# Kernel tuning notes

Measured on AMD Instinct MI355X. Metric: run time of the kernel, lower is better.

Reference implementation:

```python
import jax, jax.numpy as jnp
import numpy as np


def setup_inputs() -> dict:
    key = jax.random.key(0)
    kq, kk, kv = jax.random.split(key, 3)
    B, H, S, D = 4, 16, 2048, 64
    q = jax.random.normal(kq, (B, H, S, D), dtype=jnp.float32)
    k = jax.random.normal(kk, (B, H, S, D), dtype=jnp.float32)
    v = jax.random.normal(kv, (B, H, S, D), dtype=jnp.float32)
    return {"q": q, "k": k, "v": v}


def reference(q, k, v):
    # Flash-attention math (causal=True, softmax_scale = 1/sqrt(head_dim)).
    D = q.shape[-1]
    scale = 1.0 / np.sqrt(D).astype(np.float32)
    # scores: [B, H, Sq, Sk]
    scores = jnp.einsum('bhqd,bhkd->bhqk', q, k) * scale
    Sq, Sk = scores.shape[-2], scores.shape[-1]
    causal_mask = jnp.tril(jnp.ones((Sq, Sk), dtype=bool))  # [Sq, Sk]
    neg_inf = jnp.asarray(jnp.finfo(scores.dtype).min, scores.dtype)
    scores = jnp.where(causal_mask, scores, neg_inf)
    probs = jax.nn.softmax(scores, axis=-1)
    out = jnp.einsum('bhqk,bhkd->bhqd', probs, v)
    return out
```

## Files before the change

### kernel.cpp

```cpp
#include <hip/hip_runtime.h>
#include <hip/hip_bf16.h>

#define S_LEN 2048
#define DH 64
#define QBLK 128
#define KVBLK 64
#define LDPK 72
#define LDPV 68

typedef __attribute__((ext_vector_type(4)))  float f32x4;
typedef __attribute__((ext_vector_type(16))) float f32x16;
typedef __attribute__((ext_vector_type(8)))  short short8v;
typedef __attribute__((ext_vector_type(4)))  unsigned uint4v;
typedef __attribute__((ext_vector_type(2)))  unsigned uint2v;

__device__ __forceinline__ unsigned cvt_pk(float a, float b) {
    unsigned r;
    asm("v_cvt_pk_bf16_f32 %0, %1, %2" : "=v"(r) : "v"(a), "v"(b));
    return r;
}

__global__ __launch_bounds__(512) void fa_fwd_kernel(
    const float* __restrict__ Q, const float* __restrict__ K,
    const float* __restrict__ V, float* __restrict__ O)
{
    const int tid  = threadIdx.x;
    const int lane = tid & 63;
    const int w    = tid >> 6;
    const int bh   = blockIdx.x & 63;
    const int p    = blockIdx.x >> 6;

    const int qb = (w < 4) ? (15 - p) : p;
    const int q0 = qb * QBLK + (w & 3) * 32;
    const int kv_end = (16 - p) * QBLK;

    const size_t base = (size_t)bh * S_LEN * DH;
    const float* Qg = Q + base;
    const float* Kg = K + base;
    const float* Vg = V + base;
    float*       Og = O + base;

    __shared__ __align__(16) short K_lds[2][KVBLK][LDPK];
    __shared__ __align__(16) short V_lds[2][DH][LDPV];

    const int q  = lane & 31;
    const int hi = lane >> 5;
    const int kr = tid >> 3;
    const int dc = (tid & 7) * 8;
    const int vd = tid & 63;
    const int vg = tid >> 6;

    unsigned kpfu[4], vpf[4];

    auto prefetch = [&](int kvb) {
        const float* kp = Kg + (size_t)(kvb + kr) * DH + dc;
        f32x4 a = *(const f32x4*)kp;
        f32x4 b = *(const f32x4*)(kp + 4);
        kpfu[0] = cvt_pk(a[0], a[1]); kpfu[1] = cvt_pk(a[2], a[3]);
        kpfu[2] = cvt_pk(b[0], b[1]); kpfu[3] = cvt_pk(b[2], b[3]);
        #pragma unroll
        for (int i = 0; i < 4; ++i) {
            int kv = vg * 8 + i * 2;
            float x = Vg[(size_t)(kvb + kv) * DH + vd];
            float y = Vg[(size_t)(kvb + kv + 1) * DH + vd];
            vpf[i] = cvt_pk(x, y);
        }
    };

    auto stage = [&](int b) {
        uint4v u = {kpfu[0], kpfu[1], kpfu[2], kpfu[3]};
        *(uint4v*)&K_lds[b][kr][dc] = u;
        #pragma unroll
        for (int i = 0; i < 4; ++i) {
            int kv = vg * 8 + i * 2;
            *(unsigned*)((char*)&V_lds[b][0][0] + vd * (LDPV * 2) + kv * 2) = vpf[i];
        }
    };

    const float qscale = 0.125f * 1.44269504088896340736f;

    short8v qfrag[4];
    #pragma unroll
    for (int ds = 0; ds < 4; ++ds) {
        const float* qp = Qg + (size_t)(q0 + q) * DH + ds * 16 + hi * 8;
        f32x4 a = *(const f32x4*)qp;
        f32x4 b = *(const f32x4*)(qp + 4);
        uint4v u;
        u[0] = cvt_pk(a[0] * qscale, a[1] * qscale);
        u[1] = cvt_pk(a[2] * qscale, a[3] * qscale);
        u[2] = cvt_pk(b[0] * qscale, b[1] * qscale);
        u[3] = cvt_pk(b[2] * qscale, b[3] * qscale);
        qfrag[ds] = __builtin_bit_cast(short8v, u);
    }

    f32x16 o_acc[2];
    o_acc[0] = (f32x16)(0.f);
    o_acc[1] = (f32x16)(0.f);
    float m_run = -1e30f, l_run = 0.f;

    prefetch(0);
    stage(0);
    int cur = 0;
    __syncthreads();

    #pragma unroll 1
    for (int kvb = 0; kvb < kv_end; kvb += KVBLK) {
        int nkv = kvb + KVBLK;
        const bool have = nkv < kv_end;
        if (have) prefetch(nkv);

        if (kvb <= q0) {
            const short (*Kc)[LDPK] = K_lds[cur];
            const char* Vc = (const char*)&V_lds[cur][0][0];

            f32x16 s_acc[2];
            s_acc[0] = (f32x16)(0.f);
            s_acc[1] = (f32x16)(0.f);

            __builtin_amdgcn_s_setprio(1);
            #pragma unroll
            for (int ds = 0; ds < 4; ++ds) {
                #pragma unroll
                for (int kt = 0; kt < 2; ++kt) {
                    short8v kf = *(const short8v*)&Kc[kt * 32 + q][ds * 16 + hi * 8];
                    s_acc[kt] = __builtin_amdgcn_mfma_f32_32x32x16_bf16(
                        kf, qfrag[ds], s_acc[kt], 0, 0, 0);
                }
            }
            __builtin_amdgcn_s_setprio(0);

            const int qrow = q0 + q;
            if (kvb + KVBLK - 1 > q0) {
                #pragma unroll
                for (int kt = 0; kt < 2; ++kt)
                    #pragma unroll
                    for (int r = 0; r < 16; ++r) {
                        int kv = kvb + kt * 32 + (r & 3) + 8 * (r >> 2) + 4 * hi;
                        if (kv > qrow) s_acc[kt][r] = -1e30f;
                    }
            }

            float tl = -1e30f;
            #pragma unroll
            for (int kt = 0; kt < 2; ++kt)
                #pragma unroll
                for (int r = 0; r < 16; ++r)
                    tl = fmaxf(tl, s_acc[kt][r]);
            float tmax = fmaxf(tl, __shfl_xor(tl, 32));

            if (!__all(tmax <= m_run + 8.0f)) {
                float mnew = fmaxf(m_run, tmax);
                float corr = __builtin_amdgcn_exp2f(m_run - mnew);
                m_run = mnew;
                l_run *= corr;
                #pragma unroll
                for (int dt = 0; dt < 2; ++dt)
                    #pragma unroll
                    for (int r = 0; r < 16; ++r)
                        o_acc[dt][r] *= corr;
            }

            float rsum = 0.f;
            #pragma unroll
            for (int kt = 0; kt < 2; ++kt)
                #pragma unroll
                for (int r = 0; r < 16; ++r) {
                    float pe = __builtin_amdgcn_exp2f(s_acc[kt][r] - m_run);
                    s_acc[kt][r] = pe;
                    rsum += pe;
                }
            rsum += __shfl_xor(rsum, 32);
            l_run += rsum;

            unsigned pk_[2][8];
            #pragma unroll
            for (int kt = 0; kt < 2; ++kt)
                #pragma unroll
                for (int m = 0; m < 8; ++m)
                    pk_[kt][m] = cvt_pk(s_acc[kt][2 * m], s_acc[kt][2 * m + 1]);

            __builtin_amdgcn_s_setprio(1);
            #pragma unroll
            for (int s = 0; s < 4; ++s) {
                const int kt = s >> 1, bofs = 4 * (s & 1);
                uint4v bu = {pk_[kt][bofs], pk_[kt][bofs + 1],
                             pk_[kt][bofs + 2], pk_[kt][bofs + 3]};
                short8v pb = __builtin_bit_cast(short8v, bu);
                #pragma unroll
                for (int dt = 0; dt < 2; ++dt) {
                    const char* vrow = Vc + (size_t)(dt * 32 + q) * (LDPV * 2);
                    uint2v lo = *(const uint2v*)(vrow + (16 * s + 4 * hi) * 2);
                    uint2v h2 = *(const uint2v*)(vrow + (16 * s + 8 + 4 * hi) * 2);
                    uint4v au = {lo[0], lo[1], h2[0], h2[1]};
                    short8v va = __builtin_bit_cast(short8v, au);
                    o_acc[dt] = __builtin_amdgcn_mfma_f32_32x32x16_bf16(
                        va, pb, o_acc[dt], 0, 0, 0);
                }
            }
            __builtin_amdgcn_s_setprio(0);
        }

        if (have) {
            stage(cur ^ 1);
            __syncthreads();
        }
        cur ^= 1;
    }

    float inv = 1.0f / l_run;
    float* orow = Og + (size_t)(q0 + q) * DH;
    #pragma unroll
    for (int dt = 0; dt < 2; ++dt) {
        #pragma unroll
        for (int g = 0; g < 4; ++g) {
            f32x4 ov = {o_acc[dt][4 * g] * inv,     o_acc[dt][4 * g + 1] * inv,
                        o_acc[dt][4 * g + 2] * inv, o_acc[dt][4 * g + 3] * inv};
            *(f32x4*)(orow + dt * 32 + 8 * g + 4 * hi) = ov;
        }
    }
}

extern "C" void kernel_launch(void* const* d_in, const int* in_sizes, int n_in,
                              void* d_out, int out_size, void* d_ws, size_t ws_size,
                              hipStream_t stream) {
    const float* q = (const float*)d_in[0];
    const float* k = (const float*)d_in[1];
    const float* v = (const float*)d_in[2];
    float* out = (float*)d_out;
    fa_fwd_kernel<<<dim3(512), dim3(512), 0, stream>>>(q, k, v, out);
}
```

Before: 65.68 us.

## Permute V LDS layout for 128-bit reads, remap blocks, tree-reduce softmax

Widens the V LDS row pitch and stores V columns in a permuted order. Each MFMA A-fragment can then be fetched with a single 128-bit LDS read instead of two 64-bit reads, and staging uses two 64-bit writes instead of four 32-bit writes. The block-to-(bh, p) mapping is reordered so concurrently scheduled blocks pair light and heavy causal work differently and may share heads for cache locality. The softmax max and sum reductions become tree reductions to shorten dependency chains, at the cost of slightly more registers and a possible change in LDS bank conflicts.

```diff
diff --git a/kernel.cpp b/kernel.cpp
--- a/kernel.cpp
+++ b/kernel.cpp
@@ -6,7 +6,7 @@
 #define QBLK 128
 #define KVBLK 64
 #define LDPK 72
-#define LDPV 68
+#define LDPV 72
 
 typedef __attribute__((ext_vector_type(4)))  float f32x4;
 typedef __attribute__((ext_vector_type(16))) float f32x16;
@@ -18,6 +18,14 @@
     unsigned r;
     asm("v_cvt_pk_bf16_f32 %0, %1, %2" : "=v"(r) : "v"(a), "v"(b));
     return r;
+}
+
+__device__ __forceinline__ int vcol(int kv) {
+    int ss = kv >> 4, w16 = kv & 15;
+    int hi = (w16 >> 2) & 1;
+    int m  = w16 - 4 * hi;
+    int j  = (m & 3) + 4 * (m >> 3);
+    return ss * 16 + hi * 8 + j;
 }
 
 __global__ __launch_bounds__(512) void fa_fwd_kernel(
@@ -27,8 +35,10 @@
     const int tid  = threadIdx.x;
     const int lane = tid & 63;
     const int w    = tid >> 6;
-    const int bh   = blockIdx.x & 63;
-    const int p    = blockIdx.x >> 6;
+    const int bid  = blockIdx.x;
+    const int lo8  = (bid >> 5) & 7;
+    const int p    = (bid < 256) ? lo8 : 7 - lo8;
+    const int bh   = (bid & 31) | ((bid >> 8) << 5);
 
     const int qb = (w < 4) ? (15 - p) : p;
     const int q0 = qb * QBLK + (w & 3) * 32;
@@ -49,6 +59,8 @@
     const int dc = (tid & 7) * 8;
     const int vd = tid & 63;
     const int vg = tid >> 6;
+    const int c0 = vcol(vg * 8);
+    const int c1 = vcol(vg * 8 + 4);
 
     unsigned kpfu[4], vpf[4];
 
@@ -70,11 +82,10 @@
     auto stage = [&](int b) {
         uint4v u = {kpfu[0], kpfu[1], kpfu[2], kpfu[3]};
         *(uint4v*)&K_lds[b][kr][dc] = u;
-        #pragma unroll
-        for (int i = 0; i < 4; ++i) {
-            int kv = vg * 8 + i * 2;
-            *(unsigned*)((char*)&V_lds[b][0][0] + vd * (LDPV * 2) + kv * 2) = vpf[i];
-        }
+        uint2v v0 = {vpf[0], vpf[1]};
+        uint2v v1 = {vpf[2], vpf[3]};
+        *(uint2v*)&V_lds[b][vd][c0] = v0;
+        *(uint2v*)&V_lds[b][vd][c1] = v1;
     };
 
     const float qscale = 0.125f * 1.44269504088896340736f;
@@ -140,13 +151,16 @@
                     }
             }
 
-            float tl = -1e30f;
-            #pragma unroll
-            for (int kt = 0; kt < 2; ++kt)
-                #pragma unroll
-                for (int r = 0; r < 16; ++r)
-                    tl = fmaxf(tl, s_acc[kt][r]);
-            float tmax = fmaxf(tl, __shfl_xor(tl, 32));
+            float pm[16];
+            #pragma unroll
+            for (int r = 0; r < 16; ++r)
+                pm[r] = fmaxf(s_acc[0][r], s_acc[1][r]);
+            #pragma unroll
+            for (int st = 8; st >= 1; st >>= 1)
+                #pragma unroll
+                for (int r = 0; r < st; ++r)
+                    pm[r] = fmaxf(pm[r], pm[r + st]);
+            float tmax = fmaxf(pm[0], __shfl_xor(pm[0], 32));
 
             if (!__all(tmax <= m_run + 8.0f)) {
                 float mnew = fmaxf(m_run, tmax);
@@ -160,17 +174,21 @@
                         o_acc[dt][r] *= corr;
             }
 
-            float rsum = 0.f;
-            #pragma unroll
-            for (int kt = 0; kt < 2; ++kt)
-                #pragma unroll
-                for (int r = 0; r < 16; ++r) {
-                    float pe = __builtin_amdgcn_exp2f(s_acc[kt][r] - m_run);
-                    s_acc[kt][r] = pe;
-                    rsum += pe;
-                }
-            rsum += __shfl_xor(rsum, 32);
-            l_run += rsum;
+            float ps[16];
+            #pragma unroll
+            for (int r = 0; r < 16; ++r) {
+                float a = __builtin_amdgcn_exp2f(s_acc[0][r] - m_run);
+                float b = __builtin_amdgcn_exp2f(s_acc[1][r] - m_run);
+                s_acc[0][r] = a;
+                s_acc[1][r] = b;
+                ps[r] = a + b;
+            }
+            #pragma unroll
+            for (int st = 8; st >= 1; st >>= 1)
+                #pragma unroll
+                for (int r = 0; r < st; ++r)
+                    ps[r] += ps[r + st];
+            l_run += ps[0] + __shfl_xor(ps[0], 32);
 
             unsigned pk_[2][8];
             #pragma unroll
@@ -188,11 +206,8 @@
                 short8v pb = __builtin_bit_cast(short8v, bu);
                 #pragma unroll
                 for (int dt = 0; dt < 2; ++dt) {
-                    const char* vrow = Vc + (size_t)(dt * 32 + q) * (LDPV * 2);
-                    uint2v lo = *(const uint2v*)(vrow + (16 * s + 4 * hi) * 2);
-                    uint2v h2 = *(const uint2v*)(vrow + (16 * s + 8 + 4 * hi) * 2);
-                    uint4v au = {lo[0], lo[1], h2[0], h2[1]};
-                    short8v va = __builtin_bit_cast(short8v, au);
+                    short8v va = *(const short8v*)(Vc +
+                        (size_t)(dt * 32 + q) * (LDPV * 2) + (16 * s + 8 * hi) * 2);
                     o_acc[dt] = __builtin_amdgcn_mfma_f32_32x32x16_bf16(
                         va, pb, o_acc[dt], 0, 0, 0);
                 }
```

Measured after the change: 75.96 us. 1.16x slower.

## Split KV tiles across wave pairs and merge partial softmax states in LDS

Applied to the files above, without the earlier changes.

Doubles the grid so each block handles half of each paired Q tile. Waves are split by parity so that each wave pair processes alternating KV tiles for the same 32 query rows. The two partial (m, l, O) states are then merged through shared memory reused as a merge buffer. The aim is more parallelism and shorter per-wave serial KV loops. The cost is that every block now streams the full KV range for only half the queries, which doubles K/V global loads and LDS staging, plus an extra merge step.

```diff
diff --git a/kernel.cpp b/kernel.cpp
--- a/kernel.cpp
+++ b/kernel.cpp
@@ -28,11 +28,16 @@
     const int lane = tid & 63;
     const int w    = tid >> 6;
     const int bh   = blockIdx.x & 63;
-    const int p    = blockIdx.x >> 6;
-
-    const int qb = (w < 4) ? (15 - p) : p;
-    const int q0 = qb * QBLK + (w & 3) * 32;
+    const int pp   = blockIdx.x >> 6;
+    const int p    = pp & 7;
+    const int half = pp >> 3;
+
+    const int u    = w & 3;
+    const int par  = w >> 2;
+    const int qb   = (u < 2) ? (15 - p) : p;
+    const int q0   = qb * QBLK + half * 64 + (u & 1) * 32;
     const int kv_end = (16 - p) * QBLK;
+    const int T    = kv_end >> 6;
 
     const size_t base = (size_t)bh * S_LEN * DH;
     const float* Qg = Q + base;
@@ -40,8 +45,10 @@
     const float* Vg = V + base;
     float*       Og = O + base;
 
-    __shared__ __align__(16) short K_lds[2][KVBLK][LDPK];
-    __shared__ __align__(16) short V_lds[2][DH][LDPV];
+    __shared__ __align__(16) char smem[35840];
+    short (*K_lds)[KVBLK][LDPK] = (short(*)[KVBLK][LDPK])smem;
+    short (*V_lds)[DH][LDPV]    = (short(*)[DH][LDPV])(smem + 18432);
+    float (*Mbuf)[64][34]       = (float(*)[64][34])smem;
 
     const int q  = lane & 31;
     const int hi = lane >> 5;
@@ -68,8 +75,8 @@
     };
 
     auto stage = [&](int b) {
-        uint4v u = {kpfu[0], kpfu[1], kpfu[2], kpfu[3]};
-        *(uint4v*)&K_lds[b][kr][dc] = u;
+        uint4v uu = {kpfu[0], kpfu[1], kpfu[2], kpfu[3]};
+        *(uint4v*)&K_lds[b][kr][dc] = uu;
         #pragma unroll
         for (int i = 0; i < 4; ++i) {
             int kv = vg * 8 + i * 2;
@@ -85,12 +92,12 @@
         const float* qp = Qg + (size_t)(q0 + q) * DH + ds * 16 + hi * 8;
         f32x4 a = *(const f32x4*)qp;
         f32x4 b = *(const f32x4*)(qp + 4);
-        uint4v u;
-        u[0] = cvt_pk(a[0] * qscale, a[1] * qscale);
-        u[1] = cvt_pk(a[2] * qscale, a[3] * qscale);
-        u[2] = cvt_pk(b[0] * qscale, b[1] * qscale);
-        u[3] = cvt_pk(b[2] * qscale, b[3] * qscale);
-        qfrag[ds] = __builtin_bit_cast(short8v, u);
+        uint4v uu;
+        uu[0] = cvt_pk(a[0] * qscale, a[1] * qscale);
+        uu[1] = cvt_pk(a[2] * qscale, a[3] * qscale);
+        uu[2] = cvt_pk(b[0] * qscale, b[1] * qscale);
+        uu[3] = cvt_pk(b[2] * qscale, b[3] * qscale);
+        qfrag[ds] = __builtin_bit_cast(short8v, uu);
     }
 
     f32x16 o_acc[2];
@@ -98,107 +105,109 @@
     o_acc[1] = (f32x16)(0.f);
     float m_run = -1e30f, l_run = 0.f;
 
+    auto computeTile = [&](int cur, int kvb) {
+        const short (*Kc)[LDPK] = K_lds[cur];
+        const char* Vc = (const char*)&V_lds[cur][0][0];
+
+        f32x16 s_acc[2];
+        s_acc[0] = (f32x16)(0.f);
+        s_acc[1] = (f32x16)(0.f);
+
+        __builtin_amdgcn_s_setprio(1);
+        #pragma unroll
+        for (int ds = 0; ds < 4; ++ds) {
+            #pragma unroll
+            for (int kt = 0; kt < 2; ++kt) {
+                short8v kf = *(const short8v*)&Kc[kt * 32 + q][ds * 16 + hi * 8];
+                s_acc[kt] = __builtin_amdgcn_mfma_f32_32x32x16_bf16(
+                    kf, qfrag[ds], s_acc[kt], 0, 0, 0);
+            }
+        }
+        __builtin_amdgcn_s_setprio(0);
+
+        const int qrow = q0 + q;
+        if (kvb + KVBLK - 1 > q0) {
+            #pragma unroll
+            for (int kt = 0; kt < 2; ++kt)
+                #pragma unroll
+                for (int r = 0; r < 16; ++r) {
+                    int kv = kvb + kt * 32 + (r & 3) + 8 * (r >> 2) + 4 * hi;
+                    if (kv > qrow) s_acc[kt][r] = -1e30f;
+                }
+        }
+
+        float tl = -1e30f;
+        #pragma unroll
+        for (int kt = 0; kt < 2; ++kt)
+            #pragma unroll
+            for (int r = 0; r < 16; ++r)
+                tl = fmaxf(tl, s_acc[kt][r]);
+        float tmax = fmaxf(tl, __shfl_xor(tl, 32));
+
+        if (!__all(tmax <= m_run + 8.0f)) {
+            float mnew = fmaxf(m_run, tmax);
+            float corr = __builtin_amdgcn_exp2f(m_run - mnew);
+            m_run = mnew;
+            l_run *= corr;
+            #pragma unroll
+            for (int dt = 0; dt < 2; ++dt)
+                #pragma unroll
+                for (int r = 0; r < 16; ++r)
+                    o_acc[dt][r] *= corr;
+        }
+
+        float rsum = 0.f;
+        #pragma unroll
+        for (int kt = 0; kt < 2; ++kt)
+            #pragma unroll
+            for (int r = 0; r < 16; ++r) {
+                float pe = __builtin_amdgcn_exp2f(s_acc[kt][r] - m_run);
+                s_acc[kt][r] = pe;
+                rsum += pe;
+            }
+        rsum += __shfl_xor(rsum, 32);
+        l_run += rsum;
+
+        unsigned pk_[2][8];
+        #pragma unroll
+        for (int kt = 0; kt < 2; ++kt)
+            #pragma unroll
+            for (int m = 0; m < 8; ++m)
+                pk_[kt][m] = cvt_pk(s_acc[kt][2 * m], s_acc[kt][2 * m + 1]);
+
+        __builtin_amdgcn_s_setprio(1);
+        #pragma unroll
+        for (int ss = 0; ss < 4; ++ss) {
+            const int kt = ss >> 1, bofs = 4 * (ss & 1);
+            uint4v bu = {pk_[kt][bofs], pk_[kt][bofs + 1],
+                         pk_[kt][bofs + 2], pk_[kt][bofs + 3]};
+            short8v pb = __builtin_bit_cast(short8v, bu);
+            #pragma unroll
+            for (int dt = 0; dt < 2; ++dt) {
+                const char* vrow = Vc + (size_t)(dt * 32 + q) * (LDPV * 2);
+                uint2v lo = *(const uint2v*)(vrow + (16 * ss + 4 * hi) * 2);
+                uint2v h2 = *(const uint2v*)(vrow + (16 * ss + 8 + 4 * hi) * 2);
+                uint4v au = {lo[0], lo[1], h2[0], h2[1]};
+                short8v va = __builtin_bit_cast(short8v, au);
+                o_acc[dt] = __builtin_amdgcn_mfma_f32_32x32x16_bf16(
+                    va, pb, o_acc[dt], 0, 0, 0);
+            }
+        }
+        __builtin_amdgcn_s_setprio(0);
+    };
+
     prefetch(0);
     stage(0);
     int cur = 0;
     __syncthreads();
 
     #pragma unroll 1
-    for (int kvb = 0; kvb < kv_end; kvb += KVBLK) {
-        int nkv = kvb + KVBLK;
-        const bool have = nkv < kv_end;
-        if (have) prefetch(nkv);
-
-        if (kvb <= q0) {
-            const short (*Kc)[LDPK] = K_lds[cur];
-            const char* Vc = (const char*)&V_lds[cur][0][0];
-
-            f32x16 s_acc[2];
-            s_acc[0] = (f32x16)(0.f);
-            s_acc[1] = (f32x16)(0.f);
-
-            __builtin_amdgcn_s_setprio(1);
-            #pragma unroll
-            for (int ds = 0; ds < 4; ++ds) {
-                #pragma unroll
-                for (int kt = 0; kt < 2; ++kt) {
-                    short8v kf = *(const short8v*)&Kc[kt * 32 + q][ds * 16 + hi * 8];
-                    s_acc[kt] = __builtin_amdgcn_mfma_f32_32x32x16_bf16(
-                        kf, qfrag[ds], s_acc[kt], 0, 0, 0);
-                }
-            }
-            __builtin_amdgcn_s_setprio(0);
-
-            const int qrow = q0 + q;
-            if (kvb + KVBLK - 1 > q0) {
-                #pragma unroll
-                for (int kt = 0; kt < 2; ++kt)
-                    #pragma unroll
-                    for (int r = 0; r < 16; ++r) {
-                        int kv = kvb + kt * 32 + (r & 3) + 8 * (r >> 2) + 4 * hi;
-                        if (kv > qrow) s_acc[kt][r] = -1e30f;
-                    }
-            }
-
-            float tl = -1e30f;
-            #pragma unroll
-            for (int kt = 0; kt < 2; ++kt)
-                #pragma unroll
-                for (int r = 0; r < 16; ++r)
-                    tl = fmaxf(tl, s_acc[kt][r]);
-            float tmax = fmaxf(tl, __shfl_xor(tl, 32));
-
-            if (!__all(tmax <= m_run + 8.0f)) {
-                float mnew = fmaxf(m_run, tmax);
-                float corr = __builtin_amdgcn_exp2f(m_run - mnew);
-                m_run = mnew;
-                l_run *= corr;
-                #pragma unroll
-                for (int dt = 0; dt < 2; ++dt)
-                    #pragma unroll
-                    for (int r = 0; r < 16; ++r)
-                        o_acc[dt][r] *= corr;
-            }
-
-            float rsum = 0.f;
-            #pragma unroll
-            for (int kt = 0; kt < 2; ++kt)
-                #pragma unroll
-                for (int r = 0; r < 16; ++r) {
-                    float pe = __builtin_amdgcn_exp2f(s_acc[kt][r] - m_run);
-                    s_acc[kt][r] = pe;
-                    rsum += pe;
-                }
-            rsum += __shfl_xor(rsum, 32);
-            l_run += rsum;
-
-            unsigned pk_[2][8];
-            #pragma unroll
-            for (int kt = 0; kt < 2; ++kt)
-                #pragma unroll
-                for (int m = 0; m < 8; ++m)
-                    pk_[kt][m] = cvt_pk(s_acc[kt][2 * m], s_acc[kt][2 * m + 1]);
-
-            __builtin_amdgcn_s_setprio(1);
-            #pragma unroll
-            for (int s = 0; s < 4; ++s) {
-                const int kt = s >> 1, bofs = 4 * (s & 1);
-                uint4v bu = {pk_[kt][bofs], pk_[kt][bofs + 1],
-                             pk_[kt][bofs + 2], pk_[kt][bofs + 3]};
-                short8v pb = __builtin_bit_cast(short8v, bu);
-                #pragma unroll
-                for (int dt = 0; dt < 2; ++dt) {
-                    const char* vrow = Vc + (size_t)(dt * 32 + q) * (LDPV * 2);
-                    uint2v lo = *(const uint2v*)(vrow + (16 * s + 4 * hi) * 2);
-                    uint2v h2 = *(const uint2v*)(vrow + (16 * s + 8 + 4 * hi) * 2);
-                    uint4v au = {lo[0], lo[1], h2[0], h2[1]};
-                    short8v va = __builtin_bit_cast(short8v, au);
-                    o_acc[dt] = __builtin_amdgcn_mfma_f32_32x32x16_bf16(
-                        va, pb, o_acc[dt], 0, 0, 0);
-                }
-            }
-            __builtin_amdgcn_s_setprio(0);
-        }
+    for (int s = 0; s < T; ++s) {
+        const bool have = (s + 1) < T;
+        if (have) prefetch((s + 1) * 64);
+
+        if ((s & 1) == par && s * 64 <= q0)
+            computeTile(cur, s * 64);
 
         if (have) {
             stage(cur ^ 1);
@@ -207,15 +216,37 @@
         cur ^= 1;
     }
 
-    float inv = 1.0f / l_run;
-    float* orow = Og + (size_t)(q0 + q) * DH;
-    #pragma unroll
-    for (int dt = 0; dt < 2; ++dt) {
-        #pragma unroll
-        for (int g = 0; g < 4; ++g) {
-            f32x4 ov = {o_acc[dt][4 * g] * inv,     o_acc[dt][4 * g + 1] * inv,
-                        o_acc[dt][4 * g + 2] * inv, o_acc[dt][4 * g + 3] * inv};
-            *(f32x4*)(orow + dt * 32 + 8 * g + 4 * hi) = ov;
+    __syncthreads();
+    if (par == 1) {
+        float* mb = Mbuf[u][lane];
+        mb[0] = m_run;
+        mb[1] = l_run;
+        #pragma unroll
+        for (int dt = 0; dt < 2; ++dt)
+            #pragma unroll
+            for (int r = 0; r < 16; ++r)
+                mb[2 + dt * 16 + r] = o_acc[dt][r];
+    }
+    __syncthreads();
+    if (par == 0) {
+        const float* mb = Mbuf[u][lane];
+        float mB = mb[0], lB = mb[1];
+        float mN = fmaxf(m_run, mB);
+        float sA = __builtin_amdgcn_exp2f(m_run - mN);
+        float sB = __builtin_amdgcn_exp2f(mB - mN);
+        float inv = 1.0f / (l_run * sA + lB * sB);
+        float* orow = Og + (size_t)(q0 + q) * DH;
+        #pragma unroll
+        for (int dt = 0; dt < 2; ++dt) {
+            #pragma unroll
+            for (int g = 0; g < 4; ++g) {
+                f32x4 ov;
+                #pragma unroll
+                for (int i2 = 0; i2 < 4; ++i2)
+                    ov[i2] = (o_acc[dt][4 * g + i2] * sA +
+                              mb[2 + dt * 16 + 4 * g + i2] * sB) * inv;
+                *(f32x4*)(orow + dt * 32 + 8 * g + 4 * hi) = ov;
+            }
         }
     }
 }
@@ -227,5 +258,5 @@
     const float* k = (const float*)d_in[1];
     const float* v = (const float*)d_in[2];
     float* out = (float*)d_out;
-    fa_fwd_kernel<<<dim3(512), dim3(512), 0, stream>>>(q, k, v, out);
+    fa_fwd_kernel<<<dim3(1024), dim3(512), 0, stream>>>(q, k, v, out);
 }
```

Result: slower. 95.79 us (+45.8%).
